# Kernel tuning notes

Measured on AMD Instinct MI355X. Metric: run time of the kernel, lower is better.

The kernel has to match this reference:

```python
import jax, jax.numpy as jnp
import numpy as np

B, S, H, F, E, K = 2, 1024, 1024, 4096, 8, 2
TOPK_RATIO = 0.55
EPS = 1e-8


def _ste(x, q):
    # straight-through estimator: forward = q, backward = identity on x
    return x + jax.lax.stop_gradient(q - x)


def ternary_weight(w):
    # BitNet b1.58 absmean ternarization: W -> clip(round(W/mean|W|), -1, 1) * mean|W|
    s = jnp.maximum(jnp.mean(jnp.abs(w)), EPS)
    q = jnp.clip(jnp.round(w / s), -1.0, 1.0) * s
    return _ste(w, q)


def quant_act_int4(x):
    # per-token symmetric int4 fake-quant (range [-7, 7]) with STE
    s = jnp.maximum(jnp.max(jnp.abs(x), axis=-1, keepdims=True), EPS) / 7.0
    q = jnp.clip(jnp.round(x / s), -7.0, 7.0) * s
    return _ste(x, q)


def quant_act_topk_int8(x, ratio):
    # keep top ceil(ratio*d) values by magnitude per token, then int8 fake-quant
    d = x.shape[-1]
    k = int(np.ceil(ratio * d))
    thresh = jax.lax.top_k(jnp.abs(x), k)[0][..., -1:]
    xm = jnp.where(jnp.abs(x) >= thresh, x, 0.0)
    s = jnp.maximum(jnp.max(jnp.abs(xm), axis=-1, keepdims=True), EPS) / 127.0
    q = jnp.clip(jnp.round(xm / s), -127.0, 127.0) * s
    return _ste(xm, q)


def quant_weight_int8(w):
    # per-tensor absmax int8 fake-quant for the router (Int8Linear) with STE
    s = jnp.maximum(jnp.max(jnp.abs(w)), EPS) / 127.0
    q = jnp.clip(jnp.round(w / s), -127.0, 127.0) * s
    return _ste(w, q)


def setup_inputs() -> dict:
    key = jax.random.key(0)
    ks = jax.random.split(key, 5)
    x = jax.random.normal(ks[0], (B, S, H), jnp.float32)
    w_gate = jax.random.normal(ks[1], (E, F, H), jnp.float32) * 0.02
    w_up = jax.random.normal(ks[2], (E, F, H), jnp.float32) * 0.02
    w_down = jax.random.normal(ks[3], (E, H, F), jnp.float32) * 0.02
    w_router = jax.random.normal(ks[4], (E, H), jnp.float32) * 0.02
    return {"x": x, "w_gate": w_gate, "w_up": w_up, "w_down": w_down, "w_router": w_router}


def reference(x, w_gate, w_up, w_down, w_router):
    T = B * S
    xf = x.reshape(T, H)

    # --- router (Int8Linear, higher precision than ternary) ---
    logits = xf @ quant_weight_int8(w_router).T          # [T, E]
    probs = jax.nn.softmax(logits, axis=-1)
    gates, idx = jax.lax.top_k(probs, K)                  # [T, K]
    gates = gates / jnp.sum(gates, axis=-1, keepdims=True)
    # dense combine weights [T, E]
    comb = jnp.zeros((T, E), x.dtype).at[jnp.arange(T)[:, None], idx].set(gates)

    # --- experts: BitFFN (SwiGLU with ternary weights + quantized activations) ---
    xq = quant_act_int4(xf)                               # shared int4 input quant

    def expert(wg, wu, wd):
        g = xq @ ternary_weight(wg).T                     # [T, F]
        u = xq @ ternary_weight(wu).T                     # [T, F]
        h = jax.nn.silu(g) * u
        hq = quant_act_topk_int8(h, TOPK_RATIO)
        return hq @ ternary_weight(wd).T                  # [T, H]

    expert_out = jax.vmap(expert)(w_gate, w_up, w_down)   # [E, T, H]
    out = jnp.einsum('te,eth->th', comb, expert_out)      # gated combine
    return out.reshape(B, S, H)
```

## Files before the change

### kernel.cpp

```cpp
#include <hip/hip_runtime.h>
#include <cstdint>
#include <cstddef>


#define T_TOK 2048
#define HDIM  1024
#define FDIM  4096
#define NEXP  8
#define FH    (FDIM * HDIM)
#define KTOP  2253
#define EPSF  1e-8f
#define PPAD  5120

typedef int v4i  __attribute__((ext_vector_type(4)));
typedef int v16i __attribute__((ext_vector_type(16)));

__global__ __launch_bounds__(256) void k_wabs(const float* __restrict__ w,
                                              float* __restrict__ partials) {
  int m = blockIdx.x, blk = blockIdx.y, tid = threadIdx.x;
  const float4* p = (const float4*)(w + (size_t)m * FH + (size_t)blk * 32768) + tid;
  float s0 = 0.f, s1 = 0.f, s2 = 0.f, s3 = 0.f;
#pragma unroll
  for (int i = 0; i < 8; i++) {
    float4 a = p[(4 * i + 0) * 256];
    float4 b = p[(4 * i + 1) * 256];
    float4 c = p[(4 * i + 2) * 256];
    float4 d = p[(4 * i + 3) * 256];
    s0 += fabsf(a.x) + fabsf(a.y) + fabsf(a.z) + fabsf(a.w);
    s1 += fabsf(b.x) + fabsf(b.y) + fabsf(b.z) + fabsf(b.w);
    s2 += fabsf(c.x) + fabsf(c.y) + fabsf(c.z) + fabsf(c.w);
    s3 += fabsf(d.x) + fabsf(d.y) + fabsf(d.z) + fabsf(d.w);
  }
  float s = (s0 + s1) + (s2 + s3);
  for (int o = 32; o > 0; o >>= 1) s += __shfl_down(s, o);
  __shared__ float lds[4];
  if ((tid & 63) == 0) lds[tid >> 6] = s;
  __syncthreads();
  if (tid == 0) partials[m * 128 + blk] = lds[0] + lds[1] + lds[2] + lds[3];
}

__global__ __launch_bounds__(128) void k_scales8(const float* __restrict__ partials,
                                                 float* __restrict__ s8,
                                                 float* __restrict__ thr8) {
  int tid = threadIdx.x;
  __shared__ float acc[2];
  __shared__ float svals[8];
  for (int m = 0; m < 8; m++) {
    float v = partials[m * 128 + tid];
    for (int o = 32; o > 0; o >>= 1) v += __shfl_down(v, o);
    if ((tid & 63) == 0) acc[tid >> 6] = v;
    __syncthreads();
    if (tid == 0) svals[m] = fmaxf((acc[0] + acc[1]) / (float)FH, EPSF);
    __syncthreads();
  }
  if (tid < 8) {
    float s = svals[tid];
    s8[tid] = s;
    unsigned int lo = 0u, hi = __float_as_uint(s);
    for (int it = 0; it < 32; ++it) {
      unsigned int mid = (lo + hi) >> 1;
      if (mid == lo) break;
      if (__uint_as_float(mid) / s <= 0.5f) lo = mid; else hi = mid;
    }
    thr8[tid] = __uint_as_float(lo);
  }
}

__global__ __launch_bounds__(256) void k_router(const float* __restrict__ wr,
                                                float* __restrict__ wrq) {
  int tid = threadIdx.x;
  __shared__ float lds[4];
  __shared__ float sbc;
  float mx = 0.f;
  for (int i = tid; i < NEXP * HDIM; i += 256) mx = fmaxf(mx, fabsf(wr[i]));
  for (int o = 32; o > 0; o >>= 1) mx = fmaxf(mx, __shfl_down(mx, o));
  if ((tid & 63) == 0) lds[tid >> 6] = mx;
  __syncthreads();
  if (tid == 0)
    sbc = fmaxf(fmaxf(fmaxf(lds[0], lds[1]), fmaxf(lds[2], lds[3])), EPSF) / 127.0f;
  __syncthreads();
  float s = sbc;
  for (int i = tid; i < NEXP * HDIM; i += 256) {
    float q = fminf(fmaxf(rintf(wr[i] / s), -127.f), 127.f);
    wrq[i] = q * s;
  }
}

template <int KD, int RD>
__global__ __launch_bounds__(256) void k_pack(const float* __restrict__ w,
                                              signed char* __restrict__ q,
                                              const float* __restrict__ thr8) {
  constexpr int GR = RD / 32, CCH = KD / 32;
  int e = blockIdx.x / GR, g = blockIdx.x % GR, sl = blockIdx.y;
  float thr = thr8[e];
  __shared__ unsigned int lds[32][257];
  int tid = threadIdx.x;
  const float* wb = w + ((size_t)e * RD + (size_t)g * 32) * KD + (size_t)sl * 1024;
#pragma unroll 4
  for (int i = 0; i < 32; i++) {
    float4 v = *(const float4*)(wb + (size_t)i * KD + tid * 4);
    unsigned int b0 = (fabsf(v.x) > thr) ? ((__float_as_uint(v.x) >> 31) ? 0xFFu : 1u) : 0u;
    unsigned int b1 = (fabsf(v.y) > thr) ? ((__float_as_uint(v.y) >> 31) ? 0xFFu : 1u) : 0u;
    unsigned int b2 = (fabsf(v.z) > thr) ? ((__float_as_uint(v.z) >> 31) ? 0xFFu : 1u) : 0u;
    unsigned int b3 = (fabsf(v.w) > thr) ? ((__float_as_uint(v.w) >> 31) ? 0xFFu : 1u) : 0u;
    lds[i][tid] = b0 | (b1 << 8) | (b2 << 16) | (b3 << 24);
  }
  __syncthreads();
  size_t obase = ((size_t)(e * GR + g) * CCH + (size_t)sl * 32) * 1024;
#pragma unroll
  for (int i2 = 0; i2 < 8; i2++) {
    int mI = i2 * 256 + tid;
    int c = mI >> 6, l2 = mI & 63, ln = l2 & 31, kh = l2 >> 5;
    uint4 d = *(const uint4*)&lds[ln][c * 8 + kh * 4];
    *(uint4*)(q + obase + (size_t)c * 1024 + (size_t)l2 * 16) = d;
  }
}

__global__ __launch_bounds__(256) void k_act_router(const float* __restrict__ x,
                                                    const float* __restrict__ wrq,
                                                    signed char* __restrict__ xq,
                                                    float* __restrict__ sx,
                                                    int* __restrict__ tok_e,
                                                    float* __restrict__ tok_g,
                                                    int* __restrict__ cnt) {
  int t = blockIdx.x, tid = threadIdx.x;
  float4 xv = *(const float4*)(x + (size_t)t * HDIM + tid * 4);
  __shared__ float lds[4];
  __shared__ float sbc;
  __shared__ float part[8][256];
  __shared__ float lg[8];
  float mx = fmaxf(fmaxf(fabsf(xv.x), fabsf(xv.y)), fmaxf(fabsf(xv.z), fabsf(xv.w)));
  for (int o = 32; o > 0; o >>= 1) mx = fmaxf(mx, __shfl_down(mx, o));
  if ((tid & 63) == 0) lds[tid >> 6] = mx;
  __syncthreads();
  if (tid == 0)
    sbc = fmaxf(fmaxf(fmaxf(lds[0], lds[1]), fmaxf(lds[2], lds[3])), EPSF) / 7.0f;
  __syncthreads();
  float s = sbc;
  int q0 = (int)fminf(fmaxf(rintf(xv.x / s), -7.f), 7.f);
  int q1 = (int)fminf(fmaxf(rintf(xv.y / s), -7.f), 7.f);
  int q2 = (int)fminf(fmaxf(rintf(xv.z / s), -7.f), 7.f);
  int q3 = (int)fminf(fmaxf(rintf(xv.w / s), -7.f), 7.f);
  int packed = (q0 & 255) | ((q1 & 255) << 8) | ((q2 & 255) << 16) | (q3 << 24);
  *(int*)(xq + (size_t)t * HDIM + tid * 4) = packed;
  if (tid == 0) sx[t] = s;
#pragma unroll
  for (int e = 0; e < 8; e++) {
    float4 w = *(const float4*)(wrq + e * HDIM + tid * 4);
    part[e][tid] = xv.x * w.x + xv.y * w.y + xv.z * w.z + xv.w * w.w;
  }
  __syncthreads();
  if (tid < 8) {
    float sum = 0.f;
    for (int i = 0; i < 256; i++) sum += part[tid][i];
    lg[tid] = sum;
  }
  __syncthreads();
  if (tid == 0) {
    float m = lg[0];
    for (int e = 1; e < 8; e++) m = fmaxf(m, lg[e]);
    float p[8]; float S = 0.f;
    for (int e = 0; e < 8; e++) { p[e] = expf(lg[e] - m); S += p[e]; }
    for (int e = 0; e < 8; e++) p[e] /= S;
    int e0 = 0;
    for (int e = 1; e < 8; e++) if (p[e] > p[e0]) e0 = e;
    int e1 = -1;
    for (int e = 0; e < 8; e++) { if (e == e0) continue; if (e1 < 0 || p[e] > p[e1]) e1 = e; }
    float g0 = p[e0], g1 = p[e1], gs = g0 + g1;
    tok_e[2 * t] = e0;  tok_e[2 * t + 1] = e1;
    tok_g[2 * t] = g0 / gs;  tok_g[2 * t + 1] = g1 / gs;
    atomicAdd(&cnt[e0], 1); atomicAdd(&cnt[e1], 1);
  }
}

__global__ void k_plan(const int* __restrict__ cnt, int* __restrict__ offs,
                       int* __restrict__ tile_e, int* __restrict__ tile_m0,
                       int* __restrict__ tile_cnt) {
  if (threadIdx.x == 0 && blockIdx.x == 0) {
    int o = 0;
    for (int e = 0; e < 8; e++) { offs[e] = o; o += (cnt[e] + 127) & ~127; }
    offs[8] = o;
    int tt = 0;
    for (int e = 0; e < 8; e++)
      for (int m0 = 0; m0 < cnt[e]; m0 += 128) { tile_e[tt] = e; tile_m0[tt] = m0; tt++; }
    *tile_cnt = tt;
  }
}

__global__ __launch_bounds__(256) void k_scatter(const int* __restrict__ tok_e,
                                                 const float* __restrict__ tok_g,
                                                 const float* __restrict__ sx,
                                                 const int* __restrict__ offs,
                                                 int* __restrict__ cnt2,
                                                 int* __restrict__ pair_tok,
                                                 float* __restrict__ pair_gate,
                                                 float* __restrict__ pair_sx) {
  int t = blockIdx.x * 256 + threadIdx.x;
  if (t >= T_TOK) return;
  for (int k = 0; k < 2; k++) {
    int e = tok_e[2 * t + k];
    int pos = offs[e] + atomicAdd(&cnt2[e], 1);
    pair_tok[pos] = t;
    pair_gate[pos] = tok_g[2 * t + k];
    pair_sx[pos] = sx[t];
  }
}

__global__ __launch_bounds__(256) void k_packA(const int* __restrict__ pair_tok,
                                               const signed char* __restrict__ xq,
                                               signed char* __restrict__ xqp) {
  int idx = blockIdx.x * 256 + threadIdx.x;
  int l = idx & 63, c = (idx >> 6) & 31, pgrp = idx >> 11;
  int p = pgrp * 32 + (l & 31);
  int tok = pair_tok[p];
  const signed char* src = xq + (size_t)tok * HDIM + c * 32 + (l >> 5) * 16;
  *(int4*)(xqp + (size_t)idx * 16) = *(const int4*)src;
}

__global__ __launch_bounds__(256, 2) void k_gemm_gu(const signed char* __restrict__ xqp,
                                                    const signed char* __restrict__ wgp,
                                                    const signed char* __restrict__ wup,
                                                    const int* __restrict__ tile_e,
                                                    const int* __restrict__ tile_m0,
                                                    const int* __restrict__ tile_cnt,
                                                    const int* __restrict__ cnt,
                                                    const int* __restrict__ offs,
                                                    const float* __restrict__ pair_sx,
                                                    const float* __restrict__ s_w,
                                                    unsigned short* __restrict__ hbuf) {
  int bx = blockIdx.x;
  if (bx >= *tile_cnt) return;
  int e = tile_e[bx], m0 = tile_m0[bx];
  int cnt_e = cnt[e], pbase = offs[e];
  int tid = threadIdx.x;
  int wave = tid >> 6, lane = tid & 63, ln = lane & 31, kh = lane >> 5;
  int fgrp = blockIdx.y * 4 + wave;
  const signed char* bg = wgp + (((size_t)e * 128 + fgrp) * 32) * 1024 + lane * 16;
  const signed char* bu = wup + (((size_t)e * 128 + fgrp) * 32) * 1024 + lane * 16;
  const signed char* ap = xqp + ((size_t)((pbase + m0) >> 5) * 32) * 1024 + lane * 16;
  v16i acc[4][2] = {};
#pragma unroll 2
  for (int c = 0; c < 32; c++) {
    v4i a[4];
#pragma unroll
    for (int mg = 0; mg < 4; mg++)
      a[mg] = *(const v4i*)(ap + (size_t)(mg * 32 + c) * 1024);
    v4i b0 = *(const v4i*)(bg + (size_t)c * 1024);
    v4i b1 = *(const v4i*)(bu + (size_t)c * 1024);
#pragma unroll
    for (int mg = 0; mg < 4; mg++) {
      acc[mg][0] = __builtin_amdgcn_mfma_i32_32x32x32_i8(a[mg], b0, acc[mg][0], 0, 0, 0);
      acc[mg][1] = __builtin_amdgcn_mfma_i32_32x32x32_i8(a[mg], b1, acc[mg][1], 0, 0, 0);
    }
  }
  float sg = s_w[e], su = s_w[8 + e];
  int col = blockIdx.y * 128 + wave * 32 + ln;
#pragma unroll
  for (int mg = 0; mg < 4; mg++) {
#pragma unroll
    for (int r = 0; r < 16; r++) {
      int rr = (r & 3) + 8 * (r >> 2) + 4 * kh;
      int ml = m0 + mg * 32 + rr;
      if (ml < cnt_e) {
        int p = pbase + ml;
        float sxv = pair_sx[p];
        float gf = (float)acc[mg][0][r] * (sxv * sg);
        float uf = (float)acc[mg][1][r] * (sxv * su);
        float h = gf / (1.0f + expf(-gf)) * uf;
        ((_Float16*)hbuf)[(size_t)p * FDIM + col] = (_Float16)h;
      }
    }
  }
}

__global__ __launch_bounds__(256) void k_select(const unsigned short* __restrict__ hbuf,
                                                signed char* __restrict__ hqp,
                                                const float* __restrict__ pair_gate,
                                                float* __restrict__ pair_f) {
  int wv = threadIdx.x >> 6, lane = threadIdx.x & 63;
  int p = blockIdx.x * 4 + wv;
  const unsigned short* row = hbuf + (size_t)p * FDIM + lane * 64;
  unsigned short hs[64];
#pragma unroll
  for (int i = 0; i < 8; i++)
    *(uint4*)(hs + i * 8) = *(const uint4*)(row + i * 8);
  unsigned short ua[64];
  unsigned int mxb = 0;
#pragma unroll
  for (int j = 0; j < 64; j++) {
    unsigned int u = hs[j] & 0x7fffu;
    ua[j] = (unsigned short)u;
    mxb = (u > mxb) ? u : mxb;
  }
  for (int o = 32; o > 0; o >>= 1) {
    unsigned int t = (unsigned int)__shfl_down((int)mxb, o);
    mxb = (t > mxb) ? t : mxb;
  }
  mxb = (unsigned int)__shfl((int)mxb, 0);
  unsigned int lo = 0, hi = 0x7c00u;
  for (int it = 0; it < 15; ++it) {
    unsigned int mid = (lo + hi) >> 1;
    int cntk = 0;
#pragma unroll
    for (int j = 0; j < 64; j++)
      cntk += (int)__popcll(__ballot((unsigned int)ua[j] >= mid));
    if (cntk >= KTOP) lo = mid; else hi = mid;
  }
  unsigned int thr = lo;
  unsigned short mxs = (unsigned short)mxb;
  float smax = (float)(*(const _Float16*)&mxs);
  float sq = fmaxf(smax, EPSF) / 127.0f;
  int pgrp = p >> 5, ln = p & 31;
#pragma unroll
  for (int gj = 0; gj < 4; gj++) {
    int c = 2 * lane + (gj >> 1);
    int kh = gj & 1;
    signed char outb[16];
#pragma unroll
    for (int t = 0; t < 16; t++) {
      int j = gj * 16 + t;
      float v = (float)(((const _Float16*)hs)[j]);
      float m = ((unsigned int)ua[j] >= thr) ? v : 0.0f;
      float q = fminf(fmaxf(rintf(m / sq), -127.f), 127.f);
      outb[t] = (signed char)(int)q;
    }
    *(int4*)(hqp + ((size_t)((size_t)pgrp * 128 + c) * 64 + kh * 32 + ln) * 16) =
        *(const int4*)outb;
  }
  if (lane == 0) pair_f[p] = pair_gate[p] * sq;
}

__global__ __launch_bounds__(256, 2) void k_gemm_down(const signed char* __restrict__ hqp,
                                                      const signed char* __restrict__ wdp,
                                                      const int* __restrict__ tile_e,
                                                      const int* __restrict__ tile_m0,
                                                      const int* __restrict__ tile_cnt,
                                                      const int* __restrict__ cnt,
                                                      const int* __restrict__ offs,
                                                      const int* __restrict__ pair_tok,
                                                      const float* __restrict__ pair_f,
                                                      const float* __restrict__ s_w,
                                                      float* __restrict__ out) {
  int bx = blockIdx.x;
  if (bx >= *tile_cnt) return;
  int e = tile_e[bx], m0 = tile_m0[bx];
  int cnt_e = cnt[e], pbase = offs[e];
  int tid = threadIdx.x;
  int wave = tid >> 6, lane = tid & 63, ln = lane & 31, kh = lane >> 5;
  int ggrp = blockIdx.y * 4 + wave;
  int c0 = blockIdx.z * 64;
  const signed char* bp = wdp + (((size_t)e * 32 + ggrp) * 128) * 1024 + lane * 16;
  const signed char* ap = hqp + ((size_t)((pbase + m0) >> 5) * 128) * 1024 + lane * 16;
  v16i acc[4] = {};
#pragma unroll 4
  for (int c = c0; c < c0 + 64; c++) {
    v4i a[4];
#pragma unroll
    for (int mg = 0; mg < 4; mg++)
      a[mg] = *(const v4i*)(ap + (size_t)(mg * 128 + c) * 1024);
    v4i b = *(const v4i*)(bp + (size_t)c * 1024);
#pragma unroll
    for (int mg = 0; mg < 4; mg++)
      acc[mg] = __builtin_amdgcn_mfma_i32_32x32x32_i8(a[mg], b, acc[mg], 0, 0, 0);
  }
  float sd = s_w[16 + e];
  int col = blockIdx.y * 128 + wave * 32 + ln;
#pragma unroll
  for (int mg = 0; mg < 4; mg++) {
#pragma unroll
    for (int r = 0; r < 16; r++) {
      int rr = (r & 3) + 8 * (r >> 2) + 4 * kh;
      int ml = m0 + mg * 32 + rr;
      if (ml < cnt_e) {
        int p = pbase + ml;
        float v = (float)acc[mg][r] * (pair_f[p] * sd);
        atomicAdd(out + (size_t)pair_tok[p] * HDIM + col, v);
      }
    }
  }
}

extern "C" void kernel_launch(void* const* d_in, const int* in_sizes, int n_in,
                              void* d_out, int out_size, void* d_ws, size_t ws_size,
                              hipStream_t stream) {
  const float* x  = (const float*)d_in[0];
  const float* wg = (const float*)d_in[1];
  const float* wu = (const float*)d_in[2];
  const float* wd = (const float*)d_in[3];
  const float* wr = (const float*)d_in[4];
  float* out = (float*)d_out;
  char* ws = (char*)d_ws;
  (void)in_sizes; (void)n_in; (void)out_size; (void)ws_size;

  size_t o = 0;
  auto alloc = [&](size_t b) { size_t r = o; o += (b + 255) & ~(size_t)255; return r; };
  float* partials   = (float*)(ws + alloc(3 * 8 * 128 * 4));
  float* s_w        = (float*)(ws + alloc(24 * 4));
  float* thr_w      = (float*)(ws + alloc(24 * 4));
  float* wrq        = (float*)(ws + alloc((size_t)NEXP * HDIM * 4));
  int*   tok_e      = (int*)  (ws + alloc((size_t)T_TOK * 2 * 4));
  float* tok_g      = (float*)(ws + alloc((size_t)T_TOK * 2 * 4));
  int*   cnt        = (int*)  (ws + alloc(256));
  int*   cnt2       = cnt + 8;
  int*   offs       = (int*)  (ws + alloc(16 * 4));
  int*   tile_e     = (int*)  (ws + alloc(128 * 4));
  int*   tile_m0    = (int*)  (ws + alloc(128 * 4));
  int*   tile_cnt   = (int*)  (ws + alloc(4));
  int*   pair_tok   = (int*)  (ws + alloc((size_t)PPAD * 4));
  float* pair_gate  = (float*)(ws + alloc((size_t)PPAD * 4));
  float* pair_sx    = (float*)(ws + alloc((size_t)PPAD * 4));
  float* pair_f     = (float*)(ws + alloc((size_t)PPAD * 4));
  float* sx         = (float*)(ws + alloc((size_t)T_TOK * 4));
  signed char* xq   = (signed char*)(ws + alloc((size_t)T_TOK * HDIM));
  signed char* xqp  = (signed char*)(ws + alloc((size_t)PPAD * HDIM));
  signed char* wgp  = (signed char*)(ws + alloc((size_t)NEXP * FH));
  signed char* wup  = (signed char*)(ws + alloc((size_t)NEXP * FH));
  signed char* wdp  = (signed char*)(ws + alloc((size_t)NEXP * FH));
  unsigned short* hbuf = (unsigned short*)(ws + alloc((size_t)PPAD * FDIM * 2));
  signed char* hqp  = (signed char*)(ws + alloc((size_t)PPAD * FDIM));

  hipMemsetAsync(cnt, 0, 64, stream);
  hipMemsetAsync(pair_tok, 0, (size_t)PPAD * 4, stream);
  hipMemsetAsync(out, 0, (size_t)T_TOK * HDIM * 4, stream);

  k_wabs<<<dim3(8, 128), 256, 0, stream>>>(wg, partials);
  k_scales8<<<1, 128, 0, stream>>>(partials, s_w, thr_w);
  k_pack<1024, 4096><<<dim3(1024, 1), 256, 0, stream>>>(wg, wgp, thr_w);

  k_wabs<<<dim3(8, 128), 256, 0, stream>>>(wu, partials + 1024);
  k_scales8<<<1, 128, 0, stream>>>(partials + 1024, s_w + 8, thr_w + 8);
  k_pack<1024, 4096><<<dim3(1024, 1), 256, 0, stream>>>(wu, wup, thr_w + 8);

  k_wabs<<<dim3(8, 128), 256, 0, stream>>>(wd, partials + 2048);
  k_scales8<<<1, 128, 0, stream>>>(partials + 2048, s_w + 16, thr_w + 16);
  k_pack<4096, 1024><<<dim3(256, 4), 256, 0, stream>>>(wd, wdp, thr_w + 16);

  k_router<<<1, 256, 0, stream>>>(wr, wrq);
  k_act_router<<<T_TOK, 256, 0, stream>>>(x, wrq, xq, sx, tok_e, tok_g, cnt);
  k_plan<<<1, 64, 0, stream>>>(cnt, offs, tile_e, tile_m0, tile_cnt);
  k_scatter<<<8, 256, 0, stream>>>(tok_e, tok_g, sx, offs, cnt2, pair_tok, pair_gate, pair_sx);
  k_packA<<<PPAD / 4, 256, 0, stream>>>(pair_tok, xq, xqp);
  k_gemm_gu<<<dim3(40, 32), 256, 0, stream>>>(xqp, wgp, wup, tile_e, tile_m0, tile_cnt,
                                              cnt, offs, pair_sx, s_w, hbuf);
  k_select<<<PPAD / 4, 256, 0, stream>>>(hbuf, hqp, pair_gate, pair_f);
  k_gemm_down<<<dim3(40, 8, 2), 256, 0, stream>>>(hqp, wdp, tile_e, tile_m0, tile_cnt,
                                                  cnt, offs, pair_tok, pair_f, s_w, out);
}
```

Measured before the change: 818.7 us.

## Stage shared A tiles in LDS with double-buffered async loads in expert GEMMs

```diff
diff --git a/kernel.cpp b/kernel.cpp
--- a/kernel.cpp
+++ b/kernel.cpp
@@ -14,6 +14,12 @@
 
 typedef int v4i  __attribute__((ext_vector_type(4)));
 typedef int v16i __attribute__((ext_vector_type(16)));
+
+__device__ __forceinline__ void gload_lds16(const signed char* g, signed char* s) {
+  __builtin_amdgcn_global_load_lds((const __attribute__((address_space(1))) void*)g,
+                                   (__attribute__((address_space(3))) void*)s,
+                                   16, 0, 0);
+}
 
 __global__ __launch_bounds__(256) void k_wabs(const float* __restrict__ w,
                                               float* __restrict__ partials) {
@@ -228,6 +234,7 @@
                                                     const float* __restrict__ pair_sx,
                                                     const float* __restrict__ s_w,
                                                     unsigned short* __restrict__ hbuf) {
+  __shared__ signed char sA[2][4][8][1024];
   int bx = blockIdx.x;
   if (bx >= *tile_cnt) return;
   int e = tile_e[bx], m0 = tile_m0[bx];
@@ -237,21 +244,39 @@
   int fgrp = blockIdx.y * 4 + wave;
   const signed char* bg = wgp + (((size_t)e * 128 + fgrp) * 32) * 1024 + lane * 16;
   const signed char* bu = wup + (((size_t)e * 128 + fgrp) * 32) * 1024 + lane * 16;
-  const signed char* ap = xqp + ((size_t)((pbase + m0) >> 5) * 32) * 1024 + lane * 16;
+  const signed char* aB = xqp + ((size_t)(((pbase + m0) >> 5) + wave)) * 32768 + lane * 16;
   v16i acc[4][2] = {};
-#pragma unroll 2
-  for (int c = 0; c < 32; c++) {
-    v4i a[4];
-#pragma unroll
-    for (int mg = 0; mg < 4; mg++)
-      a[mg] = *(const v4i*)(ap + (size_t)(mg * 32 + c) * 1024);
-    v4i b0 = *(const v4i*)(bg + (size_t)c * 1024);
-    v4i b1 = *(const v4i*)(bu + (size_t)c * 1024);
-#pragma unroll
-    for (int mg = 0; mg < 4; mg++) {
-      acc[mg][0] = __builtin_amdgcn_mfma_i32_32x32x32_i8(a[mg], b0, acc[mg][0], 0, 0, 0);
-      acc[mg][1] = __builtin_amdgcn_mfma_i32_32x32x32_i8(a[mg], b1, acc[mg][1], 0, 0, 0);
-    }
+#pragma unroll
+  for (int c = 0; c < 8; c++)
+    gload_lds16(aB + (size_t)c * 1024, &sA[0][wave][c][0]);
+  int cur = 0;
+#pragma unroll
+  for (int kb = 0; kb < 4; kb++) {
+    __syncthreads();
+    v4i b0p[8], b1p[8];
+#pragma unroll
+    for (int c = 0; c < 8; c++) {
+      b0p[c] = *(const v4i*)(bg + (size_t)(kb * 8 + c) * 1024);
+      b1p[c] = *(const v4i*)(bu + (size_t)(kb * 8 + c) * 1024);
+    }
+    if (kb < 3) {
+#pragma unroll
+      for (int c = 0; c < 8; c++)
+        gload_lds16(aB + (size_t)((kb + 1) * 8 + c) * 1024, &sA[cur ^ 1][wave][c][0]);
+    }
+#pragma unroll
+    for (int c = 0; c < 8; c++) {
+      v4i a[4];
+#pragma unroll
+      for (int mg = 0; mg < 4; mg++)
+        a[mg] = *(const v4i*)&sA[cur][mg][c][lane * 16];
+#pragma unroll
+      for (int mg = 0; mg < 4; mg++) {
+        acc[mg][0] = __builtin_amdgcn_mfma_i32_32x32x32_i8(a[mg], b0p[c], acc[mg][0], 0, 0, 0);
+        acc[mg][1] = __builtin_amdgcn_mfma_i32_32x32x32_i8(a[mg], b1p[c], acc[mg][1], 0, 0, 0);
+      }
+    }
+    cur ^= 1;
   }
   float sg = s_w[e], su = s_w[8 + e];
   int col = blockIdx.y * 128 + wave * 32 + ln;
@@ -341,6 +366,7 @@
                                                       const float* __restrict__ pair_f,
                                                       const float* __restrict__ s_w,
                                                       float* __restrict__ out) {
+  __shared__ signed char sA[2][4][8][1024];
   int bx = blockIdx.x;
   if (bx >= *tile_cnt) return;
   int e = tile_e[bx], m0 = tile_m0[bx];
@@ -348,20 +374,37 @@
   int tid = threadIdx.x;
   int wave = tid >> 6, lane = tid & 63, ln = lane & 31, kh = lane >> 5;
   int ggrp = blockIdx.y * 4 + wave;
-  int c0 = blockIdx.z * 64;
+  int cbase = blockIdx.z * 64;
   const signed char* bp = wdp + (((size_t)e * 32 + ggrp) * 128) * 1024 + lane * 16;
-  const signed char* ap = hqp + ((size_t)((pbase + m0) >> 5) * 128) * 1024 + lane * 16;
+  const signed char* aB = hqp + ((size_t)(((pbase + m0) >> 5) + wave)) * 131072 + lane * 16;
   v16i acc[4] = {};
-#pragma unroll 4
-  for (int c = c0; c < c0 + 64; c++) {
-    v4i a[4];
-#pragma unroll
-    for (int mg = 0; mg < 4; mg++)
-      a[mg] = *(const v4i*)(ap + (size_t)(mg * 128 + c) * 1024);
-    v4i b = *(const v4i*)(bp + (size_t)c * 1024);
-#pragma unroll
-    for (int mg = 0; mg < 4; mg++)
-      acc[mg] = __builtin_amdgcn_mfma_i32_32x32x32_i8(a[mg], b, acc[mg], 0, 0, 0);
+#pragma unroll
+  for (int c = 0; c < 8; c++)
+    gload_lds16(aB + (size_t)(cbase + c) * 1024, &sA[0][wave][c][0]);
+  int cur = 0;
+#pragma unroll
+  for (int kb = 0; kb < 8; kb++) {
+    __syncthreads();
+    v4i bpre[8];
+#pragma unroll
+    for (int c = 0; c < 8; c++)
+      bpre[c] = *(const v4i*)(bp + (size_t)(cbase + kb * 8 + c) * 1024);
+    if (kb < 7) {
+#pragma unroll
+      for (int c = 0; c < 8; c++)
+        gload_lds16(aB + (size_t)(cbase + (kb + 1) * 8 + c) * 1024, &sA[cur ^ 1][wave][c][0]);
+    }
+#pragma unroll
+    for (int c = 0; c < 8; c++) {
+      v4i a[4];
+#pragma unroll
+      for (int mg = 0; mg < 4; mg++)
+        a[mg] = *(const v4i*)&sA[cur][mg][c][lane * 16];
+#pragma unroll
+      for (int mg = 0; mg < 4; mg++)
+        acc[mg] = __builtin_amdgcn_mfma_i32_32x32x32_i8(a[mg], bpre[c], acc[mg], 0, 0, 0);
+    }
+    cur ^= 1;
   }
   float sd = s_w[16 + e];
   int col = blockIdx.y * 128 + wave * 32 + ln;
```

Result: no change. 823.8 us (+0.6%).
